# Optimization experiments

Hardware: AMD Instinct MI355X
Metric: run time of the kernel (lower is better)

The kernel has to match this reference:

```python
import jax, jax.numpy as jnp
import numpy as np

B, S, D = 2, 1024, 4096
H, KV, HD = 32, 8, 128
GROUP = H // KV


def qlinear(x, w_int8, w_scale, bias):
    """Int8 dynamic-activation-quant linear: per-row activation scale, per-out-channel weight scale."""
    K = x.shape[-1]
    xf = x.reshape(-1, K)
    sx = jnp.max(jnp.abs(xf), axis=1, keepdims=True) / 127.0  # [M,1]
    sx = jnp.where(sx == 0, jnp.float32(1.0), sx)
    xi = jax.lax.stop_gradient(jnp.clip(jnp.round(xf / sx), -127.0, 127.0)).astype(jnp.int8)
    y = jnp.matmul(xi.astype(jnp.int32), w_int8.T.astype(jnp.int32)).astype(jnp.float32)  # int32 accum
    y = y * sx * w_scale[None, :]
    if bias is not None:
        y = y + bias
    return y.reshape(x.shape[:-1] + (w_int8.shape[0],))


def rope(t, c, s):
    half = t.shape[-1] // 2
    rot = jnp.concatenate([-t[..., half:], t[..., :half]], axis=-1)
    return t * c + rot * s


def setup_inputs() -> dict:
    key = jax.random.key(0)
    ks = jax.random.split(key, 10)
    x = jax.random.normal(ks[0], (B, S, D), dtype=jnp.float32)
    # RoPE tables (full-head_dim rotate-half convention)
    inv = 1.0 / (10000.0 ** (jnp.arange(0, HD, 2, dtype=jnp.float32) / HD))
    ang = jnp.arange(S, dtype=jnp.float32)[:, None] * inv[None, :]  # [S, HD/2]
    cos = jnp.concatenate([jnp.cos(ang), jnp.cos(ang)], axis=-1)
    sin = jnp.concatenate([jnp.sin(ang), jnp.sin(ang)], axis=-1)
    d_kv = KV * HD
    wq = jax.random.randint(ks[1], (H * HD, D), -127, 128, dtype=jnp.int32).astype(jnp.int8)
    wk = jax.random.randint(ks[2], (d_kv, D), -127, 128, dtype=jnp.int32).astype(jnp.int8)
    wv = jax.random.randint(ks[3], (d_kv, D), -127, 128, dtype=jnp.int32).astype(jnp.int8)
    wo = jax.random.randint(ks[4], (D, H * HD), -127, 128, dtype=jnp.int32).astype(jnp.int8)
    sc_in = jnp.float32(1.0 / (127.0 * np.sqrt(D)))
    sc_o = jnp.float32(1.0 / (127.0 * np.sqrt(H * HD)))
    sq = jnp.full((H * HD,), sc_in, dtype=jnp.float32)
    sk = jnp.full((d_kv,), sc_in, dtype=jnp.float32)
    sv = jnp.full((d_kv,), sc_in, dtype=jnp.float32)
    so = jnp.full((D,), sc_o, dtype=jnp.float32)
    bq = 0.01 * jax.random.normal(ks[5], (H * HD,), dtype=jnp.float32)
    bk = 0.01 * jax.random.normal(ks[6], (d_kv,), dtype=jnp.float32)
    bv = 0.01 * jax.random.normal(ks[7], (d_kv,), dtype=jnp.float32)
    return {"x": x, "cos": cos, "sin": sin, "wq": wq, "sq": sq, "bq": bq,
            "wk": wk, "sk": sk, "bk": bk, "wv": wv, "sv": sv, "bv": bv,
            "wo": wo, "so": so}


def reference(x, cos, sin, wq, sq, bq, wk, sk, bk, wv, sv, bv, wo, so):
    b, seq, _ = x.shape
    q = qlinear(x, wq, sq, bq).reshape(b, seq, H, HD)
    k = qlinear(x, wk, sk, bk).reshape(b, seq, KV, HD)
    v = qlinear(x, wv, sv, bv).reshape(b, seq, KV, HD)
    c = cos[:seq][None, :, None, :]
    s = sin[:seq][None, :, None, :]
    q = rope(q, c, s)
    k = rope(k, c, s)
    # start_pos=0 prefill: cache write then slice-back is identity -> use k, v directly.
    # GQA broadcast: q_head_to_kv_head = h // group_size
    idx = jnp.arange(H) // GROUP
    kf = k[:, :, idx, :]  # [b, seq, H, HD]
    vf = v[:, :, idx, :]
    scores = jnp.einsum('bqhd,bkhd->bhqk', q, kf) / jnp.sqrt(jnp.float32(HD))
    causal = jnp.tril(jnp.ones((seq, seq), dtype=bool))
    scores = jnp.where(causal[None, None, :, :], scores, jnp.float32(-jnp.inf))
    probs = jax.nn.softmax(scores, axis=-1)
    out = jnp.einsum('bhqk,bkhd->bqhd', probs, vf).reshape(b, seq, H * HD)
    return qlinear(out, wo, so, None)
```

## Files before the change

kernel.cpp:

```cpp
#include <hip/hip_runtime.h>


#define B_   2
#define S_   1024
#define D_   4096
#define H_   32
#define KV_  8
#define HD_  128
#define NR   (B_ * S_)
#define NQKV (H_*HD_ + 2*KV_*HD_)

typedef __attribute__((ext_vector_type(8))) short  short8;
typedef __attribute__((ext_vector_type(4))) float  f32x4;
typedef __attribute__((ext_vector_type(4))) int    int4v;

#define FA_SW(c, r) (((c) & 8) | (((c) & 7) ^ ((r) & 7)))

static __device__ __forceinline__ unsigned short f2bf(float f) {
    unsigned u = __builtin_bit_cast(unsigned, f);
    u += 0x7fffu + ((u >> 16) & 1u);
    return (unsigned short)(u >> 16);
}

static __device__ __forceinline__ void async_cp16(const void* g, void* l) {
    __builtin_amdgcn_global_load_lds(
        (const __attribute__((address_space(1))) void*)g,
        (__attribute__((address_space(3))) void*)l, 16, 0, 0);
}

__global__ __launch_bounds__(256) void quantize_rows_k(
    const float* __restrict__ X, signed char* __restrict__ Xq,
    float* __restrict__ sx_out)
{
    int row = blockIdx.x;
    const f32x4* xr = (const f32x4*)(X + (size_t)row * 4096);
    int t = threadIdx.x;

    f32x4 v[4];
    #pragma unroll
    for (int i = 0; i < 4; i++) v[i] = xr[t + i * 256];

    float m = 0.f;
    #pragma unroll
    for (int i = 0; i < 4; i++)
        #pragma unroll
        for (int j = 0; j < 4; j++) m = fmaxf(m, fabsf(v[i][j]));
    #pragma unroll
    for (int off = 32; off > 0; off >>= 1) m = fmaxf(m, __shfl_down(m, off, 64));
    __shared__ float red[4];
    if ((t & 63) == 0) red[t >> 6] = m;
    __syncthreads();
    float mm = fmaxf(fmaxf(red[0], red[1]), fmaxf(red[2], red[3]));
    float sx = mm / 127.0f;
    if (sx == 0.f) sx = 1.f;
    if (t == 0) sx_out[row] = sx;

    int* dst = (int*)(Xq + (size_t)row * 4096);
    #pragma unroll
    for (int i = 0; i < 4; i++) {
        int o = 0;
        #pragma unroll
        for (int j = 0; j < 4; j++) {
            float q = rintf(v[i][j] / sx);
            q = fminf(fmaxf(q, -127.f), 127.f);
            o |= (((int)q) & 0xff) << (j * 8);
        }
        dst[t + i * 256] = o;
    }
}

__global__ __launch_bounds__(256) void convert_all_w(
    const int* __restrict__ wq, const int* __restrict__ wk,
    const int* __restrict__ wv, const int* __restrict__ wo,
    signed char* __restrict__ Wqkv, signed char* __restrict__ Wo)
{
    int i = blockIdx.x * 256 + threadIdx.x;
    const int* src;
    int* dst;
    if (i < 4194304)      { src = wq + (size_t)i * 4;              dst = (int*)Wqkv + i; }
    else if (i < 5242880) { int j = i - 4194304; src = wk + (size_t)j * 4; dst = (int*)(Wqkv + 16777216) + j; }
    else if (i < 6291456) { int j = i - 5242880; src = wv + (size_t)j * 4; dst = (int*)(Wqkv + 20971520) + j; }
    else                  { int j = i - 6291456; src = wo + (size_t)j * 4; dst = (int*)Wo + j; }
    int4v a = *(const int4v*)src;
    *dst = (a[0] & 0xff) | ((a[1] & 0xff) << 8) | ((a[2] & 0xff) << 16) | (a[3] << 24);
}

template<int MODE>
__global__ __launch_bounds__(256) void gemm_i8_k(
    const signed char* __restrict__ A, const signed char* __restrict__ Bm,
    float* __restrict__ C, const float* __restrict__ rs,
    const float* __restrict__ cs, int K, int lda, int ldb, int ldc)
{
    __shared__ __align__(16) signed char As[128 * 128];
    __shared__ __align__(16) signed char Bs[128 * 128];

    int t    = threadIdx.x;
    int m0   = blockIdx.y * 128;
    int n0   = blockIdx.x * 128;
    int lane = t & 63;
    int w    = t >> 6;
    int wm   = (w >> 1) * 64;
    int wn   = (w & 1) * 64;
    int l15  = lane & 15;
    int quad = lane >> 4;

    int4v acc[4][4];
    #pragma unroll
    for (int i = 0; i < 4; i++)
        #pragma unroll
        for (int j = 0; j < 4; j++) { int4v z = {0,0,0,0}; acc[i][j] = z; }

    int cw   = w * 64 + lane;
    int smr  = cw >> 3;
    int scol = cw & 7;

    for (int k0 = 0; k0 < K; k0 += 128) {
        #pragma unroll
        for (int p = 0; p < 4; ++p) {
            int m  = p * 32 + smr;
            int kc = scol ^ (m & 7);
            const signed char* ga = A  + (size_t)(m0 + m) * lda + k0 + kc * 16;
            const signed char* gb = Bm + (size_t)(n0 + m) * ldb + k0 + kc * 16;
            async_cp16(ga, As + (p * 256 + w * 64) * 16);
            async_cp16(gb, Bs + (p * 256 + w * 64) * 16);
        }
        __syncthreads();

        #pragma unroll
        for (int ks = 0; ks < 2; ks++) {
            int4v af[4], bf[4];
            #pragma unroll
            for (int i = 0; i < 4; i++) {
                int ra = wm + i*16 + l15;
                int rb = wn + i*16 + l15;
                af[i] = *(const int4v*)&As[(ra * 8 + (((ks*4 + quad) ^ (ra & 7)))) * 16];
                bf[i] = *(const int4v*)&Bs[(rb * 8 + (((ks*4 + quad) ^ (rb & 7)))) * 16];
            }
            #pragma unroll
            for (int i = 0; i < 4; i++)
                #pragma unroll
                for (int j = 0; j < 4; j++)
                    acc[i][j] = __builtin_amdgcn_mfma_i32_16x16x64_i8(af[i], bf[j], acc[i][j], 0, 0, 0);
        }
        __syncthreads();
    }

    #pragma unroll
    for (int i = 0; i < 4; i++) {
        #pragma unroll
        for (int j = 0; j < 4; j++) {
            #pragma unroll
            for (int r = 0; r < 4; r++) {
                int row = m0 + wm + i*16 + quad*4 + r;
                int col = n0 + wn + j*16 + l15;
                float v = (float)acc[i][j][r];
                if (MODE == 3) v *= rs[row] * cs[col];
                C[(size_t)row * ldc + col] = v;
            }
        }
    }
}

__global__ __launch_bounds__(256) void derope_k(
    const float* __restrict__ Y, const float* __restrict__ sx,
    const float* __restrict__ sq, const float* __restrict__ bq,
    const float* __restrict__ sk, const float* __restrict__ bk,
    const float* __restrict__ sv, const float* __restrict__ bv,
    const float* __restrict__ cosb, const float* __restrict__ sinb,
    unsigned short* __restrict__ Q, unsigned short* __restrict__ Kb,
    unsigned short* __restrict__ Vt)
{
    const float qs = 0.08838834764831845f;
    int r = blockIdx.x;
    int b = r >> 10;
    int s = r & (S_ - 1);
    float sxr = sx[r];
    const float* yr = Y + (size_t)r * NQKV;
    int t = threadIdx.x;

    for (int p = t; p < H_ * 64; p += 256) {
        int h = p >> 6, d = p & 63;
        int ca = h * HD_ + d;
        float a  = yr[ca]      * sxr * sq[ca]      + bq[ca];
        float b2 = yr[ca + 64] * sxr * sq[ca + 64] + bq[ca + 64];
        float c  = cosb[s * HD_ + d], sn = sinb[s * HD_ + d];
        size_t base = (((size_t)(b * H_ + h)) * S_ + s) * HD_;
        Q[base + d]      = f2bf((a * c - b2 * sn) * qs);
        Q[base + d + 64] = f2bf((b2 * c + a * sn) * qs);
    }
    for (int p = t; p < KV_ * 64; p += 256) {
        int kv = p >> 6, d = p & 63;
        int ci = kv * HD_ + d;
        int ca = H_ * HD_ + ci;
        float a  = yr[ca]      * sxr * sk[ci]      + bk[ci];
        float b2 = yr[ca + 64] * sxr * sk[ci + 64] + bk[ci + 64];
        float c  = cosb[s * HD_ + d], sn = sinb[s * HD_ + d];
        size_t base = (((size_t)(b * KV_ + kv)) * S_ + s) * HD_;
        Kb[base + d]      = f2bf(a * c - b2 * sn);
        Kb[base + d + 64] = f2bf(b2 * c + a * sn);
    }
    for (int p = t; p < KV_ * HD_; p += 256) {
        int kv = p >> 7, d = p & 127;
        int ci = kv * HD_ + d;
        int ca = H_ * HD_ + KV_ * HD_ + ci;
        float v = yr[ca] * sxr * sv[ci] + bv[ci];
        size_t idx = (((size_t)(b * KV_ + kv)) * HD_ + d) * S_ + s;
        Vt[idx] = f2bf(v);
    }
}

__global__ __launch_bounds__(256, 2) void flash_attn_k(
    const unsigned short* __restrict__ Qg,
    const unsigned short* __restrict__ Kg,
    const unsigned short* __restrict__ Vg,
    float* __restrict__ O)
{
    __shared__ __align__(16) unsigned short Ks[128 * 128];
    __shared__ __align__(16) unsigned short Vs[128 * 128];

    int pair = blockIdx.x;
    int tp   = blockIdx.y;
    int b    = pair >> 5;
    int kv   = (pair & 31) >> 2;

    const unsigned short* Kbp = Kg + ((size_t)(b * KV_ + kv)) * (S_ * HD_);
    const unsigned short* Vb  = Vg + ((size_t)(b * KV_ + kv)) * (HD_ * S_);

    int t    = threadIdx.x;
    int lane = t & 63;
    int w    = t >> 6;
    int l15  = lane & 15;
    int quad = lane >> 4;
    int trow = t >> 4;
    int tcol = t & 15;

    short8 kreg[8], vreg[8];
    #pragma unroll
    for (int p = 0; p < 8; ++p) {
        int row = p * 16 + trow;
        kreg[p] = *(const short8*)(Kbp + (size_t)row * HD_ + tcol * 8);
        vreg[p] = *(const short8*)(Vb  + (size_t)row * S_  + tcol * 8);
    }

    #pragma unroll
    for (int phase = 0; phase < 2; ++phase) {
        int qt   = phase ? (15 - tp) : tp;
        int n128 = (qt + 2) >> 1;
        const unsigned short* Qb = Qg + ((size_t)pair * S_ + qt * 64) * HD_;

        short8 qf[4];
        #pragma unroll
        for (int ks = 0; ks < 4; ks++)
            qf[ks] = *(const short8*)(Qb + (size_t)(w*16 + l15) * HD_ + ks*32 + quad*8);

        f32x4 oacc[8];
        #pragma unroll
        for (int n = 0; n < 8; n++) { f32x4 z = {0.f,0.f,0.f,0.f}; oacc[n] = z; }
        float mrow[4], lrow[4];
        #pragma unroll
        for (int r = 0; r < 4; r++) { mrow[r] = -1e30f; lrow[r] = 0.f; }

        for (int j = 0; j < n128; ++j) {
            __syncthreads();

            #pragma unroll
            for (int p = 0; p < 8; ++p) {
                int row = p * 16 + trow;
                int c = FA_SW(tcol, row);
                *(short8*)&Ks[row * 128 + c * 8] = kreg[p];
                *(short8*)&Vs[row * 128 + c * 8] = vreg[p];
            }
            __syncthreads();

            int k0n = (j + 1 < n128) ? (j + 1) * 128 : (phase == 0 ? 0 : -1);
            if (k0n >= 0) {
                #pragma unroll
                for (int p = 0; p < 8; ++p) {
                    int row = p * 16 + trow;
                    kreg[p] = *(const short8*)(Kbp + (size_t)(k0n + row) * HD_ + tcol * 8);
                    vreg[p] = *(const short8*)(Vb  + (size_t)row * S_ + k0n + tcol * 8);
                }
            }

            f32x4 sacc[8];
            #pragma unroll
            for (int n = 0; n < 8; n++) { f32x4 z = {0.f,0.f,0.f,0.f}; sacc[n] = z; }
            #pragma unroll
            for (int n = 0; n < 8; n++) {
                int row = n*16 + l15;
                #pragma unroll
                for (int ks = 0; ks < 4; ks++) {
                    short8 kf = *(const short8*)&Ks[row * 128 + FA_SW(ks*4 + quad, row) * 8];
                    sacc[n] = __builtin_amdgcn_mfma_f32_16x16x32_bf16(qf[ks], kf, sacc[n], 0, 0, 0);
                }
            }

            if (j == n128 - 1) {
                int k0 = j * 128;
                #pragma unroll
                for (int n = 0; n < 8; n++)
                    #pragma unroll
                    for (int r = 0; r < 4; r++) {
                        int kcol = k0 + n*16 + l15;
                        int qrow = qt*64 + w*16 + quad*4 + r;
                        if (kcol > qrow) sacc[n][r] = -1e30f;
                    }
            }

            #pragma unroll
            for (int r = 0; r < 4; r++) {
                float mx = sacc[0][r];
                #pragma unroll
                for (int n = 1; n < 8; n++) mx = fmaxf(mx, sacc[n][r]);
                mx = fmaxf(mx, __shfl_xor(mx, 1, 64));
                mx = fmaxf(mx, __shfl_xor(mx, 2, 64));
                mx = fmaxf(mx, __shfl_xor(mx, 4, 64));
                mx = fmaxf(mx, __shfl_xor(mx, 8, 64));
                float mnew = fmaxf(mrow[r], mx);
                float alpha = __expf(mrow[r] - mnew);
                mrow[r] = mnew;
                float s = 0.f;
                #pragma unroll
                for (int n = 0; n < 8; n++) {
                    float e = __expf(sacc[n][r] - mnew);
                    sacc[n][r] = e;
                    s += e;
                }
                s += __shfl_xor(s, 1, 64);
                s += __shfl_xor(s, 2, 64);
                s += __shfl_xor(s, 4, 64);
                s += __shfl_xor(s, 8, 64);
                lrow[r] = lrow[r] * alpha + s;
                #pragma unroll
                for (int n = 0; n < 8; n++) oacc[n][r] *= alpha;
            }

            __syncthreads();

            #pragma unroll
            for (int n = 0; n < 8; n++)
                #pragma unroll
                for (int r = 0; r < 4; r++) {
                    int qrow = w*16 + quad*4 + r;
                    int kcol = n*16 + l15;
                    Ks[qrow * 128 + FA_SW(kcol >> 3, qrow) * 8 + (kcol & 7)] = f2bf(sacc[n][r]);
                }

            short8 pf[4];
            #pragma unroll
            for (int ks = 0; ks < 4; ks++) {
                int row = w*16 + l15;
                pf[ks] = *(const short8*)&Ks[row * 128 + FA_SW(ks*4 + quad, row) * 8];
            }
            #pragma unroll
            for (int n = 0; n < 8; n++) {
                int row = n*16 + l15;
                #pragma unroll
                for (int ks = 0; ks < 4; ks++) {
                    short8 vf = *(const short8*)&Vs[row * 128 + FA_SW(ks*4 + quad, row) * 8];
                    oacc[n] = __builtin_amdgcn_mfma_f32_16x16x32_bf16(pf[ks], vf, oacc[n], 0, 0, 0);
                }
            }
        }

        float* Ob = O + ((size_t)(b * S_ + qt * 64)) * (H_*HD_) + (pair & 31) * HD_;
        #pragma unroll
        for (int r = 0; r < 4; r++) {
            float inv = 1.0f / lrow[r];
            int row = w*16 + quad*4 + r;
            #pragma unroll
            for (int n = 0; n < 8; n++)
                Ob[(size_t)row * (H_*HD_) + n*16 + l15] = oacc[n][r] * inv;
        }
    }
}

extern "C" void kernel_launch(void* const* d_in, const int* in_sizes, int n_in,
                              void* d_out, int out_size, void* d_ws, size_t ws_size,
                              hipStream_t stream)
{
    (void)in_sizes; (void)n_in; (void)out_size; (void)ws_size;
    const float* x    = (const float*)d_in[0];
    const float* cosb = (const float*)d_in[1];
    const float* sinb = (const float*)d_in[2];
    const int*   wq   = (const int*)d_in[3];
    const float* sq   = (const float*)d_in[4];
    const float* bq   = (const float*)d_in[5];
    const int*   wk   = (const int*)d_in[6];
    const float* sk   = (const float*)d_in[7];
    const float* bk   = (const float*)d_in[8];
    const int*   wv   = (const int*)d_in[9];
    const float* sv   = (const float*)d_in[10];
    const float* bv   = (const float*)d_in[11];
    const int*   wo   = (const int*)d_in[12];
    const float* so   = (const float*)d_in[13];
    float* out = (float*)d_out;
    char*  ws  = (char*)d_ws;

    signed char*    Xi   = (signed char*)(ws + 0);
    float*          Y    = (float*)(ws + 8388608ull);
    signed char*    Wqkv = (signed char*)(ws + 58720256ull);
    signed char*    Oi   = (signed char*)(ws + 58720256ull);
    signed char*    Wo   = (signed char*)(ws + 83886080ull);
    unsigned short* Q    = (unsigned short*)(ws + 100663296ull);
    unsigned short* Kb   = (unsigned short*)(ws + 117440512ull);
    unsigned short* Vt   = (unsigned short*)(ws + 121634816ull);
    float*          O    = (float*)(ws + 125829120ull);
    float*          sx   = (float*)(ws + 159383552ull);
    float*          sxo  = (float*)(ws + 159391744ull);

    quantize_rows_k<<<dim3(NR), dim3(256), 0, stream>>>(x, Xi, sx);

    convert_all_w<<<dim3(40960), dim3(256), 0, stream>>>(wq, wk, wv, wo, Wqkv, Wo);

    gemm_i8_k<0><<<dim3(48,16,1), dim3(256), 0, stream>>>(
        Xi, Wqkv, Y, nullptr, nullptr, D_, D_, D_, NQKV);

    derope_k<<<dim3(NR), dim3(256), 0, stream>>>(
        Y, sx, sq, bq, sk, bk, sv, bv, cosb, sinb, Q, Kb, Vt);

    flash_attn_k<<<dim3(64, 8), dim3(256), 0, stream>>>(Q, Kb, Vt, O);

    quantize_rows_k<<<dim3(NR), dim3(256), 0, stream>>>(O, Oi, sxo);

    gemm_i8_k<3><<<dim3(32,16,1), dim3(256), 0, stream>>>(
        Oi, Wo, out, sxo, so, D_, D_, D_, D_);
}
```

Measured before the change: 416.0 us.

## Triple-buffer int8 GEMM with async prefetch, fragment-ordered LDS and grid swizzle

Rewrites the int8 MFMA GEMM main loop to use a 3-stage shared-memory ring with K-step 64, issuing async global-to-LDS copies three tiles ahead and waiting with explicit vmcnt counts instead of full syncthreads. LDS is laid out in MFMA fragment order, so each lane reads a contiguous 16 bytes and no XOR swizzle is needed. Block indices are remapped with an 8-way grid swizzle to improve L2 reuse, and wave priority is raised around the MFMA block. This is meant to hide global load latency behind compute. In exchange it uses 48KB of LDS, adds a second barrier per iteration, and depends on hand-tuned waitcnt values matching the async copy count.

```diff
diff --git a/kernel.cpp b/kernel.cpp
--- a/kernel.cpp
+++ b/kernel.cpp
@@ -86,64 +86,89 @@
 }
 
 template<int MODE>
-__global__ __launch_bounds__(256) void gemm_i8_k(
+__global__ __launch_bounds__(256, 3) void gemm_i8_k(
     const signed char* __restrict__ A, const signed char* __restrict__ Bm,
     float* __restrict__ C, const float* __restrict__ rs,
     const float* __restrict__ cs, int K, int lda, int ldb, int ldc)
 {
-    __shared__ __align__(16) signed char As[128 * 128];
-    __shared__ __align__(16) signed char Bs[128 * 128];
+    __shared__ __align__(16) signed char smem[3][16384];
 
     int t    = threadIdx.x;
-    int m0   = blockIdx.y * 128;
-    int n0   = blockIdx.x * 128;
     int lane = t & 63;
     int w    = t >> 6;
-    int wm   = (w >> 1) * 64;
-    int wn   = (w & 1) * 64;
     int l15  = lane & 15;
     int quad = lane >> 4;
 
+    int gx  = gridDim.x;
+    int nwg = gx * gridDim.y;
+    int lin = blockIdx.y * gx + blockIdx.x;
+    int swz = (lin & 7) * (nwg >> 3) + (lin >> 3);
+    int m0  = (swz / gx) * 128;
+    int n0  = (swz % gx) * 128;
+
+    int wm = (w >> 1) * 64;
+    int wn = (w & 1) * 64;
+
+    int ga0 = 2 * w, ga1 = 2 * w + 1;
+    const signed char* aS0 = A  + (size_t)(m0 + ga0 * 16 + l15) * lda + quad * 16;
+    const signed char* aS1 = A  + (size_t)(m0 + ga1 * 16 + l15) * lda + quad * 16;
+    const signed char* bS0 = Bm + (size_t)(n0 + ga0 * 16 + l15) * ldb + quad * 16;
+    const signed char* bS1 = Bm + (size_t)(n0 + ga1 * 16 + l15) * ldb + quad * 16;
+
+    #define STAGE(tt, cc) do {                                   \
+        int k0_ = (tt) * 64;                                     \
+        signed char* bb_ = smem[cc];                             \
+        async_cp16(aS0 + k0_, bb_ + ga0 * 1024);                 \
+        async_cp16(aS1 + k0_, bb_ + ga1 * 1024);                 \
+        async_cp16(bS0 + k0_, bb_ + 8192 + ga0 * 1024);          \
+        async_cp16(bS1 + k0_, bb_ + 8192 + ga1 * 1024);          \
+    } while (0)
+
     int4v acc[4][4];
     #pragma unroll
     for (int i = 0; i < 4; i++)
         #pragma unroll
         for (int j = 0; j < 4; j++) { int4v z = {0,0,0,0}; acc[i][j] = z; }
 
-    int cw   = w * 64 + lane;
-    int smr  = cw >> 3;
-    int scol = cw & 7;
-
-    for (int k0 = 0; k0 < K; k0 += 128) {
-        #pragma unroll
-        for (int p = 0; p < 4; ++p) {
-            int m  = p * 32 + smr;
-            int kc = scol ^ (m & 7);
-            const signed char* ga = A  + (size_t)(m0 + m) * lda + k0 + kc * 16;
-            const signed char* gb = Bm + (size_t)(n0 + m) * ldb + k0 + kc * 16;
-            async_cp16(ga, As + (p * 256 + w * 64) * 16);
-            async_cp16(gb, Bs + (p * 256 + w * 64) * 16);
+    int NT = K >> 6;
+    STAGE(0, 0);
+    STAGE(1, 1);
+    STAGE(2, 2);
+
+    int ag = (wm >> 4);
+    int bg = (wn >> 4);
+    int c = 0;
+    for (int tt = 0; tt < NT; ++tt) {
+        if (tt < NT - 2)       asm volatile("s_waitcnt vmcnt(8)" ::: "memory");
+        else if (tt == NT - 2) asm volatile("s_waitcnt vmcnt(4)" ::: "memory");
+        else                   asm volatile("s_waitcnt vmcnt(0)" ::: "memory");
+        __builtin_amdgcn_s_barrier();
+
+        const signed char* bufA = smem[c];
+        const signed char* bufB = smem[c] + 8192;
+        int4v af[4], bf[4];
+        #pragma unroll
+        for (int i = 0; i < 4; i++) {
+            af[i] = *(const int4v*)(bufA + (ag + i) * 1024 + lane * 16);
+            bf[i] = *(const int4v*)(bufB + (bg + i) * 1024 + lane * 16);
         }
-        __syncthreads();
-
-        #pragma unroll
-        for (int ks = 0; ks < 2; ks++) {
-            int4v af[4], bf[4];
-            #pragma unroll
-            for (int i = 0; i < 4; i++) {
-                int ra = wm + i*16 + l15;
-                int rb = wn + i*16 + l15;
-                af[i] = *(const int4v*)&As[(ra * 8 + (((ks*4 + quad) ^ (ra & 7)))) * 16];
-                bf[i] = *(const int4v*)&Bs[(rb * 8 + (((ks*4 + quad) ^ (rb & 7)))) * 16];
-            }
-            #pragma unroll
-            for (int i = 0; i < 4; i++)
-                #pragma unroll
-                for (int j = 0; j < 4; j++)
-                    acc[i][j] = __builtin_amdgcn_mfma_i32_16x16x64_i8(af[i], bf[j], acc[i][j], 0, 0, 0);
-        }
-        __syncthreads();
-    }
+        asm volatile("s_waitcnt lgkmcnt(0)" ::: "memory");
+        __builtin_amdgcn_s_barrier();
+
+        if (tt + 3 < NT) STAGE(tt + 3, c);
+        __builtin_amdgcn_sched_barrier(0);
+
+        __builtin_amdgcn_s_setprio(1);
+        #pragma unroll
+        for (int i = 0; i < 4; i++)
+            #pragma unroll
+            for (int j = 0; j < 4; j++)
+                acc[i][j] = __builtin_amdgcn_mfma_i32_16x16x64_i8(af[i], bf[j], acc[i][j], 0, 0, 0);
+        __builtin_amdgcn_s_setprio(0);
+
+        if (++c == 3) c = 0;
+    }
+    #undef STAGE
 
     #pragma unroll
     for (int i = 0; i < 4; i++) {
```

New measurement: 472.1 us. 1.13x slower.
